# Performance work log

Measured on AMD Instinct MI355X. Metric: run time of the kernel, lower is better.

Reference implementation:

```python
import jax, jax.numpy as jnp
import numpy as np

B, N, M, D, H = 8, 2048, 2048, 512, 8


def setup_inputs() -> dict:
    key = jax.random.key(0)
    ks = jax.random.split(key, 12)
    std = D ** (-0.5)
    inp = {
        "k": jax.random.normal(ks[0], (B, N, D), jnp.float32),
        "v": jax.random.normal(ks[1], (B, N, D), jnp.float32),
        "q": jax.random.normal(ks[2], (B, M, D), jnp.float32),
        # per-head projections, stacked over the head axis: [H, D, D]
        "Wk": jax.random.normal(ks[3], (H, D, D), jnp.float32) * std,
        "bk": jax.random.normal(ks[4], (H, D), jnp.float32) * 0.01,
        "Wv": jax.random.normal(ks[5], (H, D, D), jnp.float32) * std,
        "bv": jax.random.normal(ks[6], (H, D), jnp.float32) * 0.01,
        "Wq": jax.random.normal(ks[7], (H, D, D), jnp.float32) * std,
        "bq": jax.random.normal(ks[8], (H, D), jnp.float32) * 0.01,
        # final linear: input ordering is (hidden_dim, head) flattened -> H*D
        "Wo": jax.random.normal(ks[9], (H * D, D), jnp.float32) * (H * D) ** (-0.5),
        "bo": jax.random.normal(ks[10], (D,), jnp.float32) * 0.01,
    }
    return inp


def reference(k, v, q, Wk, bk, Wv, bv, Wq, bq, Wo, bo):
    # Per-head linear projections (torch loops over heads; here batched over h).
    # nn.Linear computes x @ W.T + b; Wk here stores W.T directly as [H, D, D].
    k_ = jnp.einsum("bnd,hde->bhne", k, Wk) + bk[None, :, None, :]  # [B,H,N,D]
    v_ = jnp.einsum("bnd,hde->bhne", v, Wv) + bv[None, :, None, :]  # [B,H,N,D]
    q_ = jnp.einsum("bmd,hde->bhme", q, Wq) + bq[None, :, None, :]  # [B,H,M,D]

    scale = D ** 0.5
    scores = jnp.einsum("bhmd,bhnd->bhmn", q_, k_) / scale  # [B,H,M,N]
    weights = jax.nn.softmax(scores, axis=-1)
    out = jnp.einsum("bhmn,bhnd->bhmd", weights, v_)  # [B,H,M,D]

    # torch: stack(outs, dim=-1) -> [B,M,D,H], then view -> [B,M,D*H]
    outs = jnp.transpose(out, (0, 2, 3, 1)).reshape(B, M, D * H)
    # matching flatten order (d-major, h-minor) requires Wo rows ordered d*H+h;
    # setup generates Wo random so any consistent ordering is faithful.
    rep = outs @ Wo + bo  # [B,M,D]
    return rep
```

## Files before the change

kernel.cpp:

```cpp
#include <hip/hip_runtime.h>
#include <hip/hip_bf16.h>
#include <cstdint>
#include <cstddef>

typedef __bf16 bf16x8 __attribute__((ext_vector_type(8)));
typedef __bf16 bf16x4 __attribute__((ext_vector_type(4)));
typedef float floatx4 __attribute__((ext_vector_type(4)));

#define MFMA16(a, b, c) __builtin_amdgcn_mfma_f32_16x16x32_bf16((a), (b), (c), 0, 0, 0)

__device__ __forceinline__ void load_lds16(const __bf16* g, __bf16* l) {
  __builtin_amdgcn_global_load_lds(
      (const __attribute__((address_space(1))) uint32_t*)(g),
      (__attribute__((address_space(3))) uint32_t*)(l), 16, 0, 0);
}

__global__ __launch_bounds__(256) void tw_t(const float* __restrict__ W,
                                            __bf16* __restrict__ Wt, float scale) {
  __shared__ float tile[64][65];
  int h = blockIdx.z, d0 = blockIdx.y * 64, e0 = blockIdx.x * 64;
  int tx = threadIdx.x & 15, ty = threadIdx.x >> 4;
  const float* src = W + ((size_t)h * 512 + d0) * 512 + e0;
#pragma unroll
  for (int j = 0; j < 4; ++j) {
    int dd = ty + j * 16;
    float4 f = *(const float4*)&src[(size_t)dd * 512 + tx * 4];
    tile[dd][tx * 4 + 0] = f.x; tile[dd][tx * 4 + 1] = f.y;
    tile[dd][tx * 4 + 2] = f.z; tile[dd][tx * 4 + 3] = f.w;
  }
  __syncthreads();
  __bf16* dst = Wt + ((size_t)h * 512 + e0) * 512 + d0;
#pragma unroll
  for (int j = 0; j < 4; ++j) {
    int ee = ty + j * 16;
    bf16x4 v;
#pragma unroll
    for (int x = 0; x < 4; ++x) v[x] = (__bf16)(tile[tx * 4 + x][ee] * scale);
    *(bf16x4*)&dst[(size_t)ee * 512 + tx * 4] = v;
  }
}

__global__ __launch_bounds__(256) void wo_t(const float* __restrict__ Wo,
                                            __bf16* __restrict__ Wot) {
  __shared__ float tile[64][65];
  int h = blockIdx.z, d0 = blockIdx.y * 64, e0 = blockIdx.x * 64;
  int tx = threadIdx.x & 15, ty = threadIdx.x >> 4;
#pragma unroll
  for (int j = 0; j < 4; ++j) {
    int dd = ty + j * 16;
    float4 f = *(const float4*)&Wo[(size_t)((d0 + dd) * 8 + h) * 512 + e0 + tx * 4];
    tile[dd][tx * 4 + 0] = f.x; tile[dd][tx * 4 + 1] = f.y;
    tile[dd][tx * 4 + 2] = f.z; tile[dd][tx * 4 + 3] = f.w;
  }
  __syncthreads();
#pragma unroll
  for (int j = 0; j < 4; ++j) {
    int ee = ty + j * 16;
    bf16x4 v;
#pragma unroll
    for (int x = 0; x < 4; ++x) v[x] = (__bf16)tile[tx * 4 + x][ee];
    *(bf16x4*)&Wot[(size_t)(e0 + ee) * 4096 + h * 512 + d0 + tx * 4] = v;
  }
}

template <int EPI, bool AF32>
__global__ __launch_bounds__(256) void gemm_bt(const void* __restrict__ Ap,
                                               const __bf16* __restrict__ Bt,
                                               const float* __restrict__ bias,
                                               void* __restrict__ Cout,
                                               int N, int K, float bscale) {
  __shared__ __align__(16) __bf16 sA[128][72];
  __shared__ __align__(16) __bf16 sB[128][72];
  const int tid = threadIdx.x;
  const int lane = tid & 63;
  const int wave = tid >> 6;
  const int lr = lane & 15;
  const int lq = lane >> 4;
  const int wm = (wave >> 1) * 64;
  const int wn = (wave & 1) * 64;
  const int bx = blockIdx.x, by = blockIdx.y;
  const int srow = tid >> 3;
  const int scol = (tid & 7) << 3;

  const floatx4 z4 = {0.f, 0.f, 0.f, 0.f};
  floatx4 acc[4][4];
#pragma unroll
  for (int i = 0; i < 4; ++i)
#pragma unroll
    for (int j = 0; j < 4; ++j) acc[i][j] = z4;

  const size_t abase = (size_t)(by * 128) * K;
  const size_t bbase = (size_t)(bx * 128) * K;

  for (int k0 = 0; k0 < K; k0 += 64) {
#pragma unroll
    for (int p = 0; p < 4; ++p) {
      int row = p * 32 + srow;
      if (AF32) {
        const float* A = (const float*)Ap;
        float4 f0 = *(const float4*)&A[abase + (size_t)row * K + k0 + scol];
        float4 f1 = *(const float4*)&A[abase + (size_t)row * K + k0 + scol + 4];
        bf16x8 v;
        v[0] = (__bf16)f0.x; v[1] = (__bf16)f0.y; v[2] = (__bf16)f0.z; v[3] = (__bf16)f0.w;
        v[4] = (__bf16)f1.x; v[5] = (__bf16)f1.y; v[6] = (__bf16)f1.z; v[7] = (__bf16)f1.w;
        *(bf16x8*)&sA[row][scol] = v;
      } else {
        const __bf16* A = (const __bf16*)Ap;
        *(bf16x8*)&sA[row][scol] = *(const bf16x8*)&A[abase + (size_t)row * K + k0 + scol];
      }
      *(bf16x8*)&sB[row][scol] = *(const bf16x8*)&Bt[bbase + (size_t)row * K + k0 + scol];
    }
    __syncthreads();
#pragma unroll
    for (int ks = 0; ks < 2; ++ks) {
      bf16x8 af[4], bfr[4];
#pragma unroll
      for (int mt = 0; mt < 4; ++mt)
        af[mt] = *(const bf16x8*)&sA[wm + mt * 16 + lr][ks * 32 + lq * 8];
#pragma unroll
      for (int nt = 0; nt < 4; ++nt)
        bfr[nt] = *(const bf16x8*)&sB[wn + nt * 16 + lr][ks * 32 + lq * 8];
#pragma unroll
      for (int mt = 0; mt < 4; ++mt)
#pragma unroll
        for (int nt = 0; nt < 4; ++nt) acc[mt][nt] = MFMA16(af[mt], bfr[nt], acc[mt][nt]);
    }
    __syncthreads();
  }

#pragma unroll
  for (int mt = 0; mt < 4; ++mt) {
#pragma unroll
    for (int nt = 0; nt < 4; ++nt) {
      int col = bx * 128 + wn + nt * 16 + lr;
      int row0 = by * 128 + wm + mt * 16 + lq * 4;
      float bcol = bias[col] * bscale;
      if (EPI == 0) {
        __bf16* dst = (__bf16*)Cout;
        int h = col >> 9, e = col & 511;
#pragma unroll
        for (int r = 0; r < 4; ++r) {
          int row = row0 + r;
          int b = row >> 11, m = row & 2047;
          dst[((size_t)((b << 3) | h) * 2048 + m) * 512 + e] = (__bf16)(acc[mt][nt][r] + bcol);
        }
      } else if (EPI == 1) {
        __bf16* dst = (__bf16*)Cout;
        int h = col >> 9, e = col & 511;
        int b = row0 >> 11, n = row0 & 2047;
        bf16x4 pk;
#pragma unroll
        for (int r = 0; r < 4; ++r) pk[r] = (__bf16)(acc[mt][nt][r] + bcol);
        *(bf16x4*)&dst[((size_t)((b << 3) | h) * 512 + e) * 2048 + n] = pk;
      } else {
        float* dst = (float*)Cout;
#pragma unroll
        for (int r = 0; r < 4; ++r) {
          int row = row0 + r;
          dst[(size_t)row * N + col] = acc[mt][nt][r] + bcol;
        }
      }
    }
  }
}

__global__ __launch_bounds__(512, 2) void attn_kernel(const __bf16* __restrict__ Qp,
                                                      const __bf16* __restrict__ Kp,
                                                      const __bf16* __restrict__ Vt,
                                                      __bf16* __restrict__ Outs) {
  __shared__ __align__(16) __bf16 kls[2][32 * 512];
  __shared__ __align__(16) __bf16 vls[2][512 * 32];
  __shared__ __align__(16) __bf16 pls[8][16 * 40];
  const int tid = threadIdx.x;
  const int lane = tid & 63;
  const int wave = tid >> 6;
  const int lr = lane & 15;
  const int lq = lane >> 4;
  const int blk = blockIdx.x;
  const int bh = blk >> 4;
  const int mblk = blk & 15;
  const int m0 = mblk * 128 + wave * 16;
  const __bf16* Qb = Qp + (size_t)bh * (2048 * 512);
  const __bf16* Kb = Kp + (size_t)bh * (2048 * 512);
  const __bf16* Vb = Vt + (size_t)bh * (512 * 2048);

  int gK[4], gV[4];
#pragma unroll
  for (int i = 0; i < 4; ++i) {
    int q = i * 512 + tid;
    int rK = q >> 6;
    gK[i] = rK * 512 + ((q & 63) ^ (rK & 7)) * 8;
    int eV = q >> 2;
    gV[i] = eV * 2048 + ((q & 3) ^ (eV & 3)) * 8;
  }

  bf16x8 qf[16];
#pragma unroll
  for (int ks = 0; ks < 16; ++ks)
    qf[ks] = *(const bf16x8*)&Qb[(size_t)(m0 + lr) * 512 + ks * 32 + lq * 8];

  const floatx4 z4 = {0.f, 0.f, 0.f, 0.f};
  floatx4 o[32];
#pragma unroll
  for (int et = 0; et < 32; ++et) o[et] = z4;
  float lsum[4] = {0.f, 0.f, 0.f, 0.f};

#pragma unroll
  for (int i = 0; i < 4; ++i) {
    load_lds16(Kb + gK[i], &kls[0][i * 4096 + wave * 512]);
    load_lds16(Vb + gV[i], &vls[0][i * 4096 + wave * 512]);
  }
  __syncthreads();

  for (int t = 0; t < 64; ++t) {
    const int cur = t & 1;
    if (t < 63) {
      const __bf16* kg = Kb + (size_t)(t + 1) * (32 * 512);
      const __bf16* vg = Vb + (t + 1) * 32;
#pragma unroll
      for (int i = 0; i < 4; ++i) {
        load_lds16(kg + gK[i], &kls[cur ^ 1][i * 4096 + wave * 512]);
        load_lds16(vg + gV[i], &vls[cur ^ 1][i * 4096 + wave * 512]);
      }
    }
    floatx4 s0 = z4, s1 = z4;
    const __bf16* kc = kls[cur];
#pragma unroll
    for (int ks = 0; ks < 16; ++ks) {
      int cidx = ((ks * 4 + lq) ^ (lr & 7)) * 8;
      bf16x8 k0 = *(const bf16x8*)&kc[lr * 512 + cidx];
      bf16x8 k1 = *(const bf16x8*)&kc[(16 + lr) * 512 + cidx];
      s0 = MFMA16(qf[ks], k0, s0);
      s1 = MFMA16(qf[ks], k1, s1);
    }
#pragma unroll
    for (int r = 0; r < 4; ++r) {
      float p0 = __expf(s0[r]);
      float p1 = __expf(s1[r]);
      lsum[r] += p0 + p1;
      pls[wave][(lq * 4 + r) * 40 + lr] = (__bf16)p0;
      pls[wave][(lq * 4 + r) * 40 + 16 + lr] = (__bf16)p1;
    }
    bf16x8 pf = *(const bf16x8*)&pls[wave][lr * 40 + lq * 8];
    const __bf16* vc = vls[cur];
#pragma unroll
    for (int et = 0; et < 32; ++et) {
      int e = et * 16 + lr;
      bf16x8 vf = *(const bf16x8*)&vc[e * 32 + ((lq ^ (e & 3)) * 8)];
      o[et] = MFMA16(pf, vf, o[et]);
    }
    __syncthreads();
  }

  float inv[4];
#pragma unroll
  for (int r = 0; r < 4; ++r) {
    float t = lsum[r];
    t += __shfl_xor(t, 1);
    t += __shfl_xor(t, 2);
    t += __shfl_xor(t, 4);
    t += __shfl_xor(t, 8);
    inv[r] = 1.0f / t;
  }
  int b = bh >> 3, h = bh & 7;
  size_t rowbase = ((size_t)b * 2048 + m0 + lq * 4) * 4096 + h * 512;
#pragma unroll
  for (int et = 0; et < 32; ++et)
#pragma unroll
    for (int r = 0; r < 4; ++r)
      Outs[rowbase + (size_t)r * 4096 + et * 16 + lr] = (__bf16)(o[et][r] * inv[r]);
}

extern "C" void kernel_launch(void* const* d_in, const int* in_sizes, int n_in,
                              void* d_out, int out_size, void* d_ws, size_t ws_size,
                              hipStream_t stream) {
  (void)in_sizes; (void)n_in; (void)out_size;
  const float* kin = (const float*)d_in[0];
  const float* vin = (const float*)d_in[1];
  const float* qin = (const float*)d_in[2];
  const float* Wk  = (const float*)d_in[3];
  const float* bk  = (const float*)d_in[4];
  const float* Wv  = (const float*)d_in[5];
  const float* bv  = (const float*)d_in[6];
  const float* Wq  = (const float*)d_in[7];
  const float* bq  = (const float*)d_in[8];
  const float* Wo  = (const float*)d_in[9];
  const float* bo  = (const float*)d_in[10];
  float* out = (float*)d_out;
  char* ws = (char*)d_ws;

  const float scale = 0.044194173824159216f;

  const size_t SZ_W = (size_t)4096 * 512 * 2;
  const size_t SZ_B = (size_t)8 * 2048 * 512 * 2;
  const size_t FIXED = 4 * SZ_W;

  int nb = 1;
  if (ws_size >= FIXED + 8 * 4 * SZ_B) nb = 8;
  else if (ws_size >= FIXED + 4 * 4 * SZ_B) nb = 4;
  else if (ws_size >= FIXED + 2 * 4 * SZ_B) nb = 2;

  __bf16* Wkt = (__bf16*)(ws);
  __bf16* Wvt = (__bf16*)(ws + SZ_W);
  __bf16* Wqt = (__bf16*)(ws + 2 * SZ_W);
  __bf16* Wot = (__bf16*)(ws + 3 * SZ_W);
  char* chunkbase = ws + FIXED;
  __bf16* kproj = (__bf16*)(chunkbase);
  __bf16* qproj = (__bf16*)(chunkbase + (size_t)nb * SZ_B);
  __bf16* vt    = (__bf16*)(chunkbase + (size_t)nb * 2 * SZ_B);
  __bf16* outs  = (__bf16*)(chunkbase + (size_t)nb * 3 * SZ_B);

  tw_t<<<dim3(8, 8, 8), dim3(256), 0, stream>>>(Wk, Wkt, 1.0f);
  tw_t<<<dim3(8, 8, 8), dim3(256), 0, stream>>>(Wv, Wvt, 1.0f);
  tw_t<<<dim3(8, 8, 8), dim3(256), 0, stream>>>(Wq, Wqt, scale);
  wo_t<<<dim3(8, 8, 8), dim3(256), 0, stream>>>(Wo, Wot);

  for (int b0 = 0; b0 < 8; b0 += nb) {
    const float* kc = kin + (size_t)b0 * 2048 * 512;
    const float* vc = vin + (size_t)b0 * 2048 * 512;
    const float* qc = qin + (size_t)b0 * 2048 * 512;
    gemm_bt<0, true><<<dim3(32, nb * 16), dim3(256), 0, stream>>>(kc, Wkt, bk, (void*)kproj, 4096, 512, 1.0f);
    gemm_bt<0, true><<<dim3(32, nb * 16), dim3(256), 0, stream>>>(qc, Wqt, bq, (void*)qproj, 4096, 512, scale);
    gemm_bt<1, true><<<dim3(32, nb * 16), dim3(256), 0, stream>>>(vc, Wvt, bv, (void*)vt, 4096, 512, 1.0f);
    attn_kernel<<<dim3(nb * 128), dim3(512), 0, stream>>>(qproj, kproj, vt, outs);
    gemm_bt<2, false><<<dim3(4, nb * 16), dim3(256), 0, stream>>>(
        (void*)outs, Wot, bo, (void*)(out + (size_t)b0 * 2048 * 512), 512, 4096, 1.0f);
  }
}
```

Before: 1.766 ms.

## Give each attention wave two 16-row query tiles to reuse K/V fragments

The attention kernel moves from 8 waves × 16 query rows to 4 waves × 32 query rows per block. Each wave now keeps two Q fragment sets and two output accumulator sets, so every K and V fragment read from LDS feeds two MFMAs. This halves LDS read traffic per MFMA. The cost is roughly double the accumulator registers (64 floatx4 outputs plus 32 Q fragments), launch bounds of (256,1), fewer waves per CU, and less latency hiding.

```diff
diff --git a/kernel.cpp b/kernel.cpp
--- a/kernel.cpp
+++ b/kernel.cpp
@@ -164,13 +164,13 @@
   }
 }
 
-__global__ __launch_bounds__(512, 2) void attn_kernel(const __bf16* __restrict__ Qp,
+__global__ __launch_bounds__(256, 1) void attn_kernel(const __bf16* __restrict__ Qp,
                                                       const __bf16* __restrict__ Kp,
                                                       const __bf16* __restrict__ Vt,
                                                       __bf16* __restrict__ Outs) {
   __shared__ __align__(16) __bf16 kls[2][32 * 512];
   __shared__ __align__(16) __bf16 vls[2][512 * 32];
-  __shared__ __align__(16) __bf16 pls[8][16 * 40];
+  __shared__ __align__(16) __bf16 pls[4][32][40];
   const int tid = threadIdx.x;
   const int lane = tid & 63;
   const int wave = tid >> 6;
@@ -179,36 +179,39 @@
   const int blk = blockIdx.x;
   const int bh = blk >> 4;
   const int mblk = blk & 15;
-  const int m0 = mblk * 128 + wave * 16;
+  const int m0 = mblk * 128 + wave * 32;
   const __bf16* Qb = Qp + (size_t)bh * (2048 * 512);
   const __bf16* Kb = Kp + (size_t)bh * (2048 * 512);
   const __bf16* Vb = Vt + (size_t)bh * (512 * 2048);
 
-  int gK[4], gV[4];
-#pragma unroll
-  for (int i = 0; i < 4; ++i) {
-    int q = i * 512 + tid;
+  int gK[8], gV[8];
+#pragma unroll
+  for (int i = 0; i < 8; ++i) {
+    int q = i * 256 + tid;
     int rK = q >> 6;
     gK[i] = rK * 512 + ((q & 63) ^ (rK & 7)) * 8;
     int eV = q >> 2;
     gV[i] = eV * 2048 + ((q & 3) ^ (eV & 3)) * 8;
   }
 
-  bf16x8 qf[16];
-#pragma unroll
-  for (int ks = 0; ks < 16; ++ks)
-    qf[ks] = *(const bf16x8*)&Qb[(size_t)(m0 + lr) * 512 + ks * 32 + lq * 8];
+  bf16x8 qf0[16], qf1[16];
+#pragma unroll
+  for (int ks = 0; ks < 16; ++ks) {
+    qf0[ks] = *(const bf16x8*)&Qb[(size_t)(m0 + lr) * 512 + ks * 32 + lq * 8];
+    qf1[ks] = *(const bf16x8*)&Qb[(size_t)(m0 + 16 + lr) * 512 + ks * 32 + lq * 8];
+  }
 
   const floatx4 z4 = {0.f, 0.f, 0.f, 0.f};
-  floatx4 o[32];
-#pragma unroll
-  for (int et = 0; et < 32; ++et) o[et] = z4;
-  float lsum[4] = {0.f, 0.f, 0.f, 0.f};
-
-#pragma unroll
-  for (int i = 0; i < 4; ++i) {
-    load_lds16(Kb + gK[i], &kls[0][i * 4096 + wave * 512]);
-    load_lds16(Vb + gV[i], &vls[0][i * 4096 + wave * 512]);
+  floatx4 o0[32], o1[32];
+#pragma unroll
+  for (int et = 0; et < 32; ++et) { o0[et] = z4; o1[et] = z4; }
+  float lsum0[4] = {0.f, 0.f, 0.f, 0.f};
+  float lsum1[4] = {0.f, 0.f, 0.f, 0.f};
+
+#pragma unroll
+  for (int i = 0; i < 8; ++i) {
+    load_lds16(Kb + gK[i], &kls[0][i * 2048 + wave * 512]);
+    load_lds16(Vb + gV[i], &vls[0][i * 2048 + wave * 512]);
   }
   __syncthreads();
 
@@ -218,57 +221,71 @@
       const __bf16* kg = Kb + (size_t)(t + 1) * (32 * 512);
       const __bf16* vg = Vb + (t + 1) * 32;
 #pragma unroll
-      for (int i = 0; i < 4; ++i) {
-        load_lds16(kg + gK[i], &kls[cur ^ 1][i * 4096 + wave * 512]);
-        load_lds16(vg + gV[i], &vls[cur ^ 1][i * 4096 + wave * 512]);
+      for (int i = 0; i < 8; ++i) {
+        load_lds16(kg + gK[i], &kls[cur ^ 1][i * 2048 + wave * 512]);
+        load_lds16(vg + gV[i], &vls[cur ^ 1][i * 2048 + wave * 512]);
       }
     }
-    floatx4 s0 = z4, s1 = z4;
+    floatx4 s00 = z4, s01 = z4, s10 = z4, s11 = z4;
     const __bf16* kc = kls[cur];
 #pragma unroll
     for (int ks = 0; ks < 16; ++ks) {
       int cidx = ((ks * 4 + lq) ^ (lr & 7)) * 8;
       bf16x8 k0 = *(const bf16x8*)&kc[lr * 512 + cidx];
       bf16x8 k1 = *(const bf16x8*)&kc[(16 + lr) * 512 + cidx];
-      s0 = MFMA16(qf[ks], k0, s0);
-      s1 = MFMA16(qf[ks], k1, s1);
+      s00 = MFMA16(qf0[ks], k0, s00);
+      s10 = MFMA16(qf1[ks], k0, s10);
+      s01 = MFMA16(qf0[ks], k1, s01);
+      s11 = MFMA16(qf1[ks], k1, s11);
     }
 #pragma unroll
     for (int r = 0; r < 4; ++r) {
-      float p0 = __expf(s0[r]);
-      float p1 = __expf(s1[r]);
-      lsum[r] += p0 + p1;
-      pls[wave][(lq * 4 + r) * 40 + lr] = (__bf16)p0;
-      pls[wave][(lq * 4 + r) * 40 + 16 + lr] = (__bf16)p1;
-    }
-    bf16x8 pf = *(const bf16x8*)&pls[wave][lr * 40 + lq * 8];
+      float p00 = __expf(s00[r]);
+      float p01 = __expf(s01[r]);
+      float p10 = __expf(s10[r]);
+      float p11 = __expf(s11[r]);
+      lsum0[r] += p00 + p01;
+      lsum1[r] += p10 + p11;
+      pls[wave][lq * 4 + r][lr] = (__bf16)p00;
+      pls[wave][lq * 4 + r][16 + lr] = (__bf16)p01;
+      pls[wave][16 + lq * 4 + r][lr] = (__bf16)p10;
+      pls[wave][16 + lq * 4 + r][16 + lr] = (__bf16)p11;
+    }
+    bf16x8 pf0 = *(const bf16x8*)&pls[wave][lr][lq * 8];
+    bf16x8 pf1 = *(const bf16x8*)&pls[wave][16 + lr][lq * 8];
     const __bf16* vc = vls[cur];
 #pragma unroll
     for (int et = 0; et < 32; ++et) {
       int e = et * 16 + lr;
       bf16x8 vf = *(const bf16x8*)&vc[e * 32 + ((lq ^ (e & 3)) * 8)];
-      o[et] = MFMA16(pf, vf, o[et]);
+      o0[et] = MFMA16(pf0, vf, o0[et]);
+      o1[et] = MFMA16(pf1, vf, o1[et]);
     }
     __syncthreads();
   }
 
-  float inv[4];
+  float inv0[4], inv1[4];
 #pragma unroll
   for (int r = 0; r < 4; ++r) {
-    float t = lsum[r];
-    t += __shfl_xor(t, 1);
-    t += __shfl_xor(t, 2);
-    t += __shfl_xor(t, 4);
-    t += __shfl_xor(t, 8);
-    inv[r] = 1.0f / t;
+    float t0 = lsum0[r];
+    t0 += __shfl_xor(t0, 1); t0 += __shfl_xor(t0, 2);
+    t0 += __shfl_xor(t0, 4); t0 += __shfl_xor(t0, 8);
+    inv0[r] = 1.0f / t0;
+    float t1 = lsum1[r];
+    t1 += __shfl_xor(t1, 1); t1 += __shfl_xor(t1, 2);
+    t1 += __shfl_xor(t1, 4); t1 += __shfl_xor(t1, 8);
+    inv1[r] = 1.0f / t1;
   }
   int b = bh >> 3, h = bh & 7;
-  size_t rowbase = ((size_t)b * 2048 + m0 + lq * 4) * 4096 + h * 512;
+  size_t rb0 = ((size_t)b * 2048 + m0 + lq * 4) * 4096 + h * 512;
+  size_t rb1 = ((size_t)b * 2048 + m0 + 16 + lq * 4) * 4096 + h * 512;
 #pragma unroll
   for (int et = 0; et < 32; ++et)
 #pragma unroll
-    for (int r = 0; r < 4; ++r)
-      Outs[rowbase + (size_t)r * 4096 + et * 16 + lr] = (__bf16)(o[et][r] * inv[r]);
+    for (int r = 0; r < 4; ++r) {
+      Outs[rb0 + (size_t)r * 4096 + et * 16 + lr] = (__bf16)(o0[et][r] * inv0[r]);
+      Outs[rb1 + (size_t)r * 4096 + et * 16 + lr] = (__bf16)(o1[et][r] * inv1[r]);
+    }
 }
 
 extern "C" void kernel_launch(void* const* d_in, const int* in_sizes, int n_in,
@@ -322,7 +339,7 @@
     gemm_bt<0, true><<<dim3(32, nb * 16), dim3(256), 0, stream>>>(kc, Wkt, bk, (void*)kproj, 4096, 512, 1.0f);
     gemm_bt<0, true><<<dim3(32, nb * 16), dim3(256), 0, stream>>>(qc, Wqt, bq, (void*)qproj, 4096, 512, scale);
     gemm_bt<1, true><<<dim3(32, nb * 16), dim3(256), 0, stream>>>(vc, Wvt, bv, (void*)vt, 4096, 512, 1.0f);
-    attn_kernel<<<dim3(nb * 128), dim3(512), 0, stream>>>(qproj, kproj, vt, outs);
+    attn_kernel<<<dim3(nb * 128), dim3(256), 0, stream>>>(qproj, kproj, vt, outs);
     gemm_bt<2, false><<<dim3(4, nb * 16), dim3(256), 0, stream>>>(
         (void*)outs, Wot, bo, (void*)(out + (size_t)b0 * 2048 * 512), 512, 4096, 1.0f);
   }
```

Result: no change. 1.778 ms (+0.7%).
